# Optimization experiments

Hardware: AMD Instinct MI355X
Metric: run time of the kernel (lower is better)

Reference implementation:

```python
import jax, jax.numpy as jnp
import numpy as np

H, W, D = 56, 56, 28            # input_resolution
WS = (7, 7, 7)                  # window size (Wh, Ww, Wd)
SS = (3, 3, 3)                  # shift size
DIM = 96
NH = 3
HD = DIM // NH
N = WS[0] * WS[1] * WS[2]       # 343 tokens per window
NW = (H // WS[0]) * (W // WS[1]) * (D // WS[2])  # 256 windows


def _rel_pos_index():
    Wd, Wh, Ww = WS
    coords = np.stack(np.meshgrid(np.arange(Wd), np.arange(Wh), np.arange(Ww), indexing='ij'))
    cf = coords.reshape(3, -1)
    rel = (cf[:, :, None] - cf[:, None, :]).transpose(1, 2, 0)
    rel[:, :, 0] += Wd - 1
    rel[:, :, 1] += Wh - 1
    rel[:, :, 2] += Ww - 1
    rel[:, :, 0] *= (2 * Wh - 1) * (2 * Ww - 1)
    rel[:, :, 1] *= (2 * Ww - 1)
    return rel.sum(-1)  # (N, N)


def _attn_mask():
    img = np.zeros((H, W, D), np.float32)
    def slices(w, s):
        return (slice(0, -w), slice(-w, -s), slice(-s, None))
    cnt = 0
    for hs in slices(WS[0], SS[0]):
        for ws in slices(WS[1], SS[1]):
            for ds in slices(WS[2], SS[2]):
                img[hs, ws, ds] = cnt
                cnt += 1
    mw = img.reshape(H // WS[0], WS[0], W // WS[1], WS[1], D // WS[2], WS[2])
    mw = mw.transpose(0, 2, 4, 1, 3, 5).reshape(-1, N)  # (NW, N)
    am = mw[:, None, :] - mw[:, :, None]
    return np.where(am != 0, np.float32(-100.0), np.float32(0.0))


REL_IDX = jnp.asarray(_rel_pos_index())
ATTN_MASK = jnp.asarray(_attn_mask())  # (NW, N, N)


def _ln(x, g, b, eps=1e-5):
    m = x.mean(-1, keepdims=True)
    v = jnp.mean((x - m) ** 2, -1, keepdims=True)
    return (x - m) * jax.lax.rsqrt(v + eps) * g + b


def _forward(x, n1g, n1b, qkv_w, qkv_b, rpb, proj_w, proj_b,
             n2g, n2b, fc1_w, fc1_b, fc2_w, fc2_b):
    B, L, C = x.shape
    shortcut = x
    h = _ln(x, n1g, n1b).reshape(B, H, W, D, C)
    # cyclic shift
    h = jnp.roll(h, (-SS[0], -SS[1], -SS[2]), axis=(1, 2, 3))
    # window partition -> (B*NW, N, C)
    h = h.reshape(B, H // WS[0], WS[0], W // WS[1], WS[1], D // WS[2], WS[2], C)
    h = h.transpose(0, 1, 3, 5, 2, 4, 6, 7).reshape(-1, N, C)
    # qkv
    qkv = (h @ qkv_w + qkv_b).reshape(-1, N, 3, NH, HD).transpose(2, 0, 3, 1, 4)
    q, k, v = qkv[0] * (HD ** -0.5), qkv[1], qkv[2]  # (B*NW, NH, N, HD)
    attn = jnp.einsum('bhnd,bhmd->bhnm', q, k)
    bias = rpb[REL_IDX.reshape(-1)].reshape(N, N, NH).transpose(2, 0, 1)
    attn = attn + bias[None]
    # shifted-window mask
    attn = attn.reshape(B, NW, NH, N, N) + ATTN_MASK[None, :, None]
    attn = jax.nn.softmax(attn.reshape(-1, NH, N, N), axis=-1)
    o = jnp.einsum('bhnm,bhmd->bhnd', attn, v).transpose(0, 2, 1, 3).reshape(-1, N, C)
    o = o @ proj_w + proj_b
    # window reverse
    o = o.reshape(B, H // WS[0], W // WS[1], D // WS[2], WS[0], WS[1], WS[2], C)
    o = o.transpose(0, 1, 4, 2, 5, 3, 6, 7).reshape(B, H, W, D, C)
    o = jnp.roll(o, SS, axis=(1, 2, 3)).reshape(B, L, C)
    x = shortcut + o
    h2 = _ln(x, n2g, n2b)
    h2 = jax.nn.gelu(h2 @ fc1_w + fc1_b, approximate=False) @ fc2_w + fc2_b
    return x + h2


def setup_inputs() -> dict:
    key = jax.random.key(0)
    ks = jax.random.split(key, 6)
    C, FF = DIM, 4 * DIM
    f32 = jnp.float32
    return {
        'x': jax.random.normal(ks[0], (1, H * W * D, C), f32),
        'n1g': jnp.ones((C,), f32), 'n1b': jnp.zeros((C,), f32),
        'qkv_w': jax.random.normal(ks[1], (C, 3 * C), f32) * 0.02,
        'qkv_b': jnp.zeros((3 * C,), f32),
        'rpb': jax.random.normal(ks[2], ((2 * WS[0] - 1) * (2 * WS[1] - 1) * (2 * WS[2] - 1), NH), f32) * 0.02,
        'proj_w': jax.random.normal(ks[3], (C, C), f32) * 0.02,
        'proj_b': jnp.zeros((C,), f32),
        'n2g': jnp.ones((C,), f32), 'n2b': jnp.zeros((C,), f32),
        'fc1_w': jax.random.normal(ks[4], (C, FF), f32) * 0.02,
        'fc1_b': jnp.zeros((FF,), f32),
        'fc2_w': jax.random.normal(ks[5], (FF, C), f32) * 0.02,
        'fc2_b': jnp.zeros((C,), f32),
    }


def reference(x, n1g, n1b, qkv_w, qkv_b, rpb, proj_w, proj_b,
              n2g, n2b, fc1_w, fc1_b, fc2_w, fc2_b):
    return _forward(x, n1g, n1b, qkv_w, qkv_b, rpb, proj_w, proj_b,
                    n2g, n2b, fc1_w, fc1_b, fc2_w, fc2_b)
```

## Files before the change

kernel.cpp:

```cpp
#include <hip/hip_runtime.h>
#include <hip/hip_bf16.h>


#define L_TOK 87808

typedef unsigned int uint;
typedef __attribute__((ext_vector_type(8))) short short8;
typedef __attribute__((ext_vector_type(4))) float f32x4;

__device__ __forceinline__ float bflo(uint u){ union{uint x; float f;} a; a.x = u << 16; return a.f; }
__device__ __forceinline__ float bfhi(uint u){ union{uint x; float f;} a; a.x = u & 0xffff0000u; return a.f; }
__device__ __forceinline__ float bfval(unsigned short w){ union{uint x; float f;} a; a.x = (uint)w << 16; return a.f; }
__device__ __forceinline__ unsigned short f2bfbits(float f){
  union{float f; uint u;} a; a.f = f;
  uint u = a.u;
  u += 0x7fffu + ((u >> 16) & 1u);
  return (unsigned short)(u >> 16);
}
__device__ __forceinline__ unsigned short bfb(float f){
  __hip_bfloat16 h = __float2bfloat16(f);
  return *reinterpret_cast<unsigned short*>(&h);
}
__device__ __forceinline__ uint pkbf(float a, float b){
  return ((uint)bfb(b) << 16) | (uint)bfb(a);
}
__device__ __forceinline__ uint pack2(float a, float b){
  return ((uint)f2bfbits(b) << 16) | (uint)f2bfbits(a);
}
__device__ __forceinline__ uint4 pack8(const float* p){
  uint4 u;
  u.x = pack2(p[0], p[1]); u.y = pack2(p[2], p[3]);
  u.z = pack2(p[4], p[5]); u.w = pack2(p[6], p[7]);
  return u;
}
__device__ __forceinline__ uint4 pack8g(const float* gp){
  float t[8];
  *(float4*)&t[0] = *(const float4*)gp;
  *(float4*)&t[4] = *(const float4*)(gp + 4);
  return pack8(t);
}

__global__ __launch_bounds__(256)
void k_tr(const float* __restrict__ src, unsigned short* __restrict__ dst,
          int K, int N)
{
  const int idx = blockIdx.x * 256 + threadIdx.x;
  if (idx < K * N) {
    const int n = idx / K, k = idx % K;
    dst[idx] = f2bfbits(src[(size_t)k * N + n]);
  }
}

__global__ __launch_bounds__(256)
void k_mb(const float* __restrict__ rpbg, unsigned short* __restrict__ MB)
{
  const int idx = blockIdx.x * 256 + threadIdx.x;
  const int cls = idx / (3*352*352);
  const int rem = idx - cls * (3*352*352);
  const int h = rem / (352*352);
  const int rem2 = rem - h * (352*352);
  const int q = rem2 / 352;
  const int k = rem2 - q * 352;
  unsigned short v = 0xFF80;
  if (q < 343 && k < 343) {
    const int q0 = q/49, q1 = (q%49)/7, q2 = q%7;
    const int k0 = k/49, k1 = (k%49)/7, k2 = k%7;
    const int bq = q0*169 + q1*13 + q2;
    const int bk = k0*169 + k1*13 + k2;
    float bias = rpbg[(size_t)(bq - bk + 1098)*3 + h];
    int cq = 0, ck = 0;
    if (cls & 4) { cq += ((q0 < 4) ? 1 : 2)*9; ck += ((k0 < 4) ? 1 : 2)*9; }
    if (cls & 2) { cq += ((q1 < 4) ? 1 : 2)*3; ck += ((k1 < 4) ? 1 : 2)*3; }
    if (cls & 1) { cq += (q2 < 4) ? 1 : 2;     ck += (k2 < 4) ? 1 : 2; }
    if (cq != ck) bias -= 100.0f;
    v = f2bfbits(bias);
  }
  MB[idx] = v;
}

__global__ __launch_bounds__(256)
void k_qkv_ln(const float* __restrict__ x,
              const float* __restrict__ n1g,
              const float* __restrict__ n1b,
              const unsigned short* __restrict__ qkvwt,
              const float* __restrict__ bias, size_t headStride,
              __hip_bfloat16* __restrict__ qb,
              __hip_bfloat16* __restrict__ kb,
              __hip_bfloat16* __restrict__ vb)
{
  __shared__ __align__(16) unsigned short As[64][104];
  __shared__ uint srcOff[64];
  __shared__ float gLds[96], bLds[96];
  __shared__ float pSum[256], pSq[256];
  __shared__ float mLds[64], sLds[64];

  const int tid = threadIdx.x;
  const int wave = tid >> 6, lane = tid & 63;
  const int row0 = blockIdx.x * 64;
  const int h = (int)blockIdx.y;
  __hip_bfloat16* qh = qb + (size_t)h * headStride;
  __hip_bfloat16* kh = kb + (size_t)h * headStride;
  __hip_bfloat16* vh = vb + (size_t)h * headStride;

  if (tid < 64) {
    const uint row = (uint)(row0 + tid);
    const uint win = row / 343u, n = row % 343u;
    const uint wh = win >> 5, ww = (win >> 2) & 7u, wd = win & 3u;
    const uint ih = n / 49u, rr = n % 49u, iw = rr / 7u, id = rr % 7u;
    uint gh = wh*7u + ih + 3u; if (gh >= 56u) gh -= 56u;
    uint gw = ww*7u + iw + 3u; if (gw >= 56u) gw -= 56u;
    uint gd = wd*7u + id + 3u; if (gd >= 28u) gd -= 28u;
    srcOff[tid] = ((gh*56u + gw)*28u + gd) * 96u;
  }
  if (tid < 96) { gLds[tid] = n1g[tid]; bLds[tid] = n1b[tid]; }
  __syncthreads();

  for (int i = tid; i < 768; i += 256) {
    const int r = i / 12, kk = (i % 12) * 8;
    *(uint4*)&As[r][kk] = pack8g(x + srcOff[r] + kk);
  }
  __syncthreads();

  {
    const int r = tid & 63, seg = tid >> 6;
    float s = 0.0f, sq = 0.0f;
    #pragma unroll
    for (int j = 0; j < 24; ++j) {
      const float v = bfval(As[r][seg*24 + j]);
      s += v; sq += v*v;
    }
    pSum[tid] = s; pSq[tid] = sq;
  }
  __syncthreads();
  if (tid < 64) {
    const float s  = pSum[tid] + pSum[tid+64] + pSum[tid+128] + pSum[tid+192];
    const float sq = pSq[tid] + pSq[tid+64] + pSq[tid+128] + pSq[tid+192];
    const float mean = s * (1.0f/96.0f);
    mLds[tid] = mean;
    sLds[tid] = rsqrtf(sq*(1.0f/96.0f) - mean*mean + 1e-5f);
  }
  __syncthreads();
  for (int i = tid; i < 768; i += 256) {
    const int r = i / 12, kk = (i % 12) * 8;
    uint4 u = *(uint4*)&As[r][kk];
    const float m = mLds[r], sc = sLds[r];
    float v[8];
    v[0]=bflo(u.x); v[1]=bfhi(u.x); v[2]=bflo(u.y); v[3]=bfhi(u.y);
    v[4]=bflo(u.z); v[5]=bfhi(u.z); v[6]=bflo(u.w); v[7]=bfhi(u.w);
    #pragma unroll
    for (int j = 0; j < 8; ++j) v[j] = (v[j] - m)*sc*gLds[kk+j] + bLds[kk+j];
    *(uint4*)&As[r][kk] = pack8(v);
  }
  __syncthreads();

  f32x4 acc[6];
  #pragma unroll
  for (int i = 0; i < 6; ++i) acc[i] = (f32x4){0.f, 0.f, 0.f, 0.f};
  const int ml = lane & 15, q8 = (lane >> 4) * 8;
  #pragma unroll
  for (int nt = 0; nt < 6; ++nt) {
    const int col = nt*16 + ml;
    const int wcol = (col >> 5)*96 + h*32 + (col & 31);
    #pragma unroll
    for (int kc = 0; kc < 3; ++kc) {
      const short8 a = *(const short8*)&As[wave*16 + ml][kc*32 + q8];
      const short8 b = *(const short8*)(qkvwt + (size_t)wcol*96 + kc*32 + q8);
      acc[nt] = __builtin_amdgcn_mfma_f32_16x16x32_bf16(a, b, acc[nt], 0, 0, 0);
    }
  }

  const float qscale = 0.17677669529663687f;
  #pragma unroll
  for (int r = 0; r < 4; ++r) {
    const size_t row = (size_t)(row0 + wave*16 + (lane >> 4)*4 + r);
    #pragma unroll
    for (int nt = 0; nt < 6; ++nt) {
      const int col = nt*16 + ml;
      const int part = col >> 5, d = col & 31;
      float v = acc[nt][r] + bias[part*96 + h*32 + d];
      if (part == 0) v *= qscale;
      __hip_bfloat16* dst = (part == 0) ? qh : ((part == 1) ? kh : vh);
      dst[row*32 + d] = __float2bfloat16(v);
    }
  }
}

__global__ __launch_bounds__(256, 4)
void k_attn_v10(const __hip_bfloat16* __restrict__ qg,
                const __hip_bfloat16* __restrict__ kg,
                const __hip_bfloat16* __restrict__ vg,
                size_t headStride,
                const unsigned short* __restrict__ MB,
                float* __restrict__ ob)
{
  __shared__ __align__(16) unsigned short vt[32*344 + 16];
  __shared__ __align__(16) unsigned short Pc[4][16*56];
  __shared__ float lred[4][16];

  const int tid = threadIdx.x;
  const int wave = tid >> 6, lane = tid & 63;
  const uint win = blockIdx.x;
  const int hh = (int)blockIdx.y;
  const int mtBase = (int)blockIdx.z * 11;
  const size_t wbase = (size_t)hh * headStride + (size_t)win * (343*32);
  const unsigned short* qw = (const unsigned short*)qg + wbase;
  const unsigned short* kw = (const unsigned short*)kg + wbase;
  const unsigned short* vw = (const unsigned short*)vg + wbase;

  const uint wh = win >> 5, ww = (win >> 2) & 7u, wd = win & 3u;
  const int cls = ((wh == 7u) ? 4 : 0) | ((ww == 7u) ? 2 : 0) | ((wd == 3u) ? 1 : 0);
  const unsigned short* MBh = MB + ((size_t)cls*3 + hh) * (352*352);

  for (int t = tid; t < 343; t += 256) {
    const uint4* src = (const uint4*)(vw + (size_t)t*32);
    #pragma unroll
    for (int c4 = 0; c4 < 4; ++c4) {
      const uint4 u = src[c4];
      const int d = c4*8;
      vt[(d+0)*344 + t] = (unsigned short)(u.x & 0xffffu);
      vt[(d+1)*344 + t] = (unsigned short)(u.x >> 16);
      vt[(d+2)*344 + t] = (unsigned short)(u.y & 0xffffu);
      vt[(d+3)*344 + t] = (unsigned short)(u.y >> 16);
      vt[(d+4)*344 + t] = (unsigned short)(u.z & 0xffffu);
      vt[(d+5)*344 + t] = (unsigned short)(u.z >> 16);
      vt[(d+6)*344 + t] = (unsigned short)(u.w & 0xffffu);
      vt[(d+7)*344 + t] = (unsigned short)(u.w >> 16);
    }
  }
  if (tid < 32) vt[tid*344 + 343] = 0;
  if (tid < 16) vt[32*344 + tid] = 0;
  __syncthreads();

  const int ml = lane & 15, g = lane >> 4, g8 = g*8;
  unsigned short* Pw = &Pc[wave][0];

  for (int mt = mtBase + wave; mt < mtBase + 11; mt += 4) {
    const int q = mt*16 + ml;
    const short8 qf = *(const short8*)(qw + (size_t)q*32 + g8);
    const unsigned short* MBq = MBh + (size_t)q * 352;
    float l = 0.0f;
    f32x4 o0 = {0.f,0.f,0.f,0.f}, o1 = {0.f,0.f,0.f,0.f};

    for (int kc = 0; kc < 11; ++kc) {
      const short8 kf0 = *(const short8*)(kw + (size_t)(kc*32 + ml)*32 + g8);
      const short8 kf1 = *(const short8*)(kw + (size_t)(kc*32 + 16 + ml)*32 + g8);
      f32x4 s0 = __builtin_amdgcn_mfma_f32_16x16x32_bf16(kf0, qf, (f32x4){0.f,0.f,0.f,0.f}, 0, 0, 0);
      f32x4 s1 = __builtin_amdgcn_mfma_f32_16x16x32_bf16(kf1, qf, (f32x4){0.f,0.f,0.f,0.f}, 0, 0, 0);

      const ushort4 u0 = *(const ushort4*)(MBq + kc*32 + 4*g);
      const ushort4 u1 = *(const ushort4*)(MBq + kc*32 + 16 + 4*g);

      float p0 = __expf(s0[0] + bfval(u0.x));
      float p1 = __expf(s0[1] + bfval(u0.y));
      float p2 = __expf(s0[2] + bfval(u0.z));
      float p3 = __expf(s0[3] + bfval(u0.w));
      float p4 = __expf(s1[0] + bfval(u1.x));
      float p5 = __expf(s1[1] + bfval(u1.y));
      float p6 = __expf(s1[2] + bfval(u1.z));
      float p7 = __expf(s1[3] + bfval(u1.w));
      l += ((p0 + p1) + (p2 + p3)) + ((p4 + p5) + (p6 + p7));

      uint2 wlo, whi;
      wlo.x = pkbf(p0, p1); wlo.y = pkbf(p2, p3);
      whi.x = pkbf(p4, p5); whi.y = pkbf(p6, p7);
      *(uint2*)&Pw[ml*56 + 4*g]      = wlo;
      *(uint2*)&Pw[ml*56 + 16 + 4*g] = whi;

      const short8 pf  = *(const short8*)&Pw[ml*56 + g8];
      const short8 vf0 = *(const short8*)&vt[(size_t)ml*344 + kc*32 + g8];
      const short8 vf1 = *(const short8*)&vt[(size_t)(16 + ml)*344 + kc*32 + g8];
      o0 = __builtin_amdgcn_mfma_f32_16x16x32_bf16(pf, vf0, o0, 0, 0, 0);
      o1 = __builtin_amdgcn_mfma_f32_16x16x32_bf16(pf, vf1, o1, 0, 0, 0);
    }

    l += __shfl_xor(l, 16);
    l += __shfl_xor(l, 32);
    if (g == 0) lred[wave][ml] = 1.0f / l;
    const float4 li = *(const float4*)&lred[wave][4*g];
    #pragma unroll
    for (int r = 0; r < 4; ++r) {
      const int row = mt*16 + 4*g + r;
      if (row < 343) {
        float* op = ob + ((size_t)win*343 + (uint)row)*96 + hh*32;
        op[ml]      = o0[r] * li[r];
        op[16 + ml] = o1[r] * li[r];
      }
    }
  }
}

__global__ __launch_bounds__(256, 4)
void k_attn_v9(const __hip_bfloat16* __restrict__ qg,
               const __hip_bfloat16* __restrict__ kg,
               const __hip_bfloat16* __restrict__ vg,
               size_t headStride,
               const float* __restrict__ rpbg,
               float* __restrict__ ob)
{
  __shared__ __align__(16) unsigned short vt[32*344 + 16];
  __shared__ __align__(16) unsigned short Pc[4][16*40];
  __shared__ short baseT[352];
  __shared__ unsigned char cntT[352];
  __shared__ unsigned short rpB[2197];

  const int tid = threadIdx.x;
  const int wave = tid >> 6, lane = tid & 63;
  const uint win = blockIdx.x;
  const int hh = (int)blockIdx.y;
  const int mtBase = (int)blockIdx.z * 11;
  const size_t wbase = (size_t)hh * headStride + (size_t)win * (343*32);
  const unsigned short* qw = (const unsigned short*)qg + wbase;
  const unsigned short* kw = (const unsigned short*)kg + wbase;
  const unsigned short* vw = (const unsigned short*)vg + wbase;

  for (int i = tid; i < 2197; i += 256) rpB[i] = f2bfbits(rpbg[i*3 + hh]);
  const uint wh = win >> 5, ww = (win >> 2) & 7u, wd = win & 3u;
  for (int i = tid; i < 352; i += 256) {
    if (i < 343) {
      const uint c0 = (uint)i/49u, rr = (uint)i%49u, c1 = rr/7u, c2 = rr%7u;
      baseT[i] = (short)(c0*169u + c1*13u + c2);
      const uint g0 = wh*7u + c0, g1 = ww*7u + c1, g2 = wd*7u + c2;
      const uint rh = (g0 < 49u) ? 0u : ((g0 < 53u) ? 1u : 2u);
      const uint rw = (g1 < 49u) ? 0u : ((g1 < 53u) ? 1u : 2u);
      const uint rd = (g2 < 21u) ? 0u : ((g2 < 25u) ? 1u : 2u);
      cntT[i] = (unsigned char)(rh*9u + rw*3u + rd);
    } else { baseT[i] = 0; cntT[i] = 255; }
  }
  for (int t = tid; t < 343; t += 256) {
    const uint4* src = (const uint4*)(vw + (size_t)t*32);
    #pragma unroll
    for (int c4 = 0; c4 < 4; ++c4) {
      const uint4 u = src[c4];
      const int d = c4*8;
      vt[(d+0)*344 + t] = (unsigned short)(u.x & 0xffffu);
      vt[(d+1)*344 + t] = (unsigned short)(u.x >> 16);
      vt[(d+2)*344 + t] = (unsigned short)(u.y & 0xffffu);
      vt[(d+3)*344 + t] = (unsigned short)(u.y >> 16);
      vt[(d+4)*344 + t] = (unsigned short)(u.z & 0xffffu);
      vt[(d+5)*344 + t] = (unsigned short)(u.z >> 16);
      vt[(d+6)*344 + t] = (unsigned short)(u.w & 0xffffu);
      vt[(d+7)*344 + t] = (unsigned short)(u.w >> 16);
    }
  }
  if (tid < 32) vt[tid*344 + 343] = 0;
  if (tid < 16) vt[32*344 + tid] = 0;
  __syncthreads();

  const int ml = lane & 15, g = lane >> 4, g8 = g*8;
  unsigned short* Pw = &Pc[wave][0];

  for (int mt = mtBase + wave; mt < mtBase + 11; mt += 4) {
    const int qrow = mt*16;
    const short8 qf = *(const short8*)(qw + (size_t)(qrow + ml)*32 + g8);
    int cnR[4], biR[4];
    #pragma unroll
    for (int r = 0; r < 4; ++r) {
      const int gi = qrow + g*4 + r;
      cnR[r] = (int)cntT[gi];
      biR[r] = (int)baseT[gi] + 1098;
    }
    float m_[4], l_[4];
    #pragma unroll
    for (int r = 0; r < 4; ++r) { m_[r] = -1e30f; l_[r] = 0.0f; }
    f32x4 o0 = {0.f,0.f,0.f,0.f}, o1 = {0.f,0.f,0.f,0.f};

    for (int kc = 0; kc < 11; ++kc) {
      const int c0 = kc*32 + ml, c1 = c0 + 16;
      const short8 kf0 = *(const short8*)(kw + (size_t)c0*32 + g8);
      const short8 kf1 = *(const short8*)(kw + (size_t)c1*32 + g8);
      f32x4 s0 = __builtin_amdgcn_mfma_f32_16x16x32_bf16(qf, kf0, (f32x4){0.f,0.f,0.f,0.f}, 0, 0, 0);
      f32x4 s1 = __builtin_amdgcn_mfma_f32_16x16x32_bf16(qf, kf1, (f32x4){0.f,0.f,0.f,0.f}, 0, 0, 0);

      float bv0[4], bv1[4];
      const int bj0 = (int)baseT[c0], bj1 = (int)baseT[c1];
      #pragma unroll
      for (int r = 0; r < 4; ++r) {
        bv0[r] = bfval(rpB[biR[r] - bj0]);
        bv1[r] = bfval(rpB[biR[r] - bj1]);
      }
      const int cj0 = (int)cntT[c0], cj1 = (int)cntT[c1];

      float a_[4];
      #pragma unroll
      for (int r = 0; r < 4; ++r) {
        float v0 = s0[r] + bv0[r];
        float v1 = s1[r] + bv1[r];
        v0 += (cj0 == cnR[r]) ? 0.0f : -100.0f;
        v1 += (cj1 == cnR[r]) ? 0.0f : -100.0f;
        v1 = (c1 < 343) ? v1 : -1e30f;
        s0[r] = v0; s1[r] = v1;
        float cm = fmaxf(v0, v1);
        cm = fmaxf(cm, __shfl_xor(cm, 1));
        cm = fmaxf(cm, __shfl_xor(cm, 2));
        cm = fmaxf(cm, __shfl_xor(cm, 4));
        cm = fmaxf(cm, __shfl_xor(cm, 8));
        const float mn = fmaxf(m_[r], cm);
        a_[r] = __expf(m_[r] - mn);
        m_[r] = mn;
      }
      #pragma unroll
      for (int r = 0; r < 4; ++r) {
        const float p0 = __expf(s0[r] - m_[r]);
        const float p1 = __expf(s1[r] - m_[r]);
        Pw[(g*4 + r)*40 + ml]      = f2bfbits(p0);
        Pw[(g*4 + r)*40 + 16 + ml] = f2bfbits(p1);
        float cs = p0 + p1;
        cs += __shfl_xor(cs, 1);
        cs += __shfl_xor(cs, 2);
        cs += __shfl_xor(cs, 4);
        cs += __shfl_xor(cs, 8);
        l_[r] = l_[r]*a_[r] + cs;
        o0[r] *= a_[r];
        o1[r] *= a_[r];
      }
      const short8 pf  = *(const short8*)&Pw[ml*40 + g8];
      const short8 vf0 = *(const short8*)&vt[(size_t)ml*344 + kc*32 + g8];
      const short8 vf1 = *(const short8*)&vt[(size_t)(16 + ml)*344 + kc*32 + g8];
      o0 = __builtin_amdgcn_mfma_f32_16x16x32_bf16(pf, vf0, o0, 0, 0, 0);
      o1 = __builtin_amdgcn_mfma_f32_16x16x32_bf16(pf, vf1, o1, 0, 0, 0);
    }

    #pragma unroll
    for (int r = 0; r < 4; ++r) {
      const int row = qrow + g*4 + r;
      if (row < 343) {
        const float inv = 1.0f / l_[r];
        float* op = ob + ((size_t)win*343 + (uint)row)*96 + hh*32;
        op[ml]      = o0[r] * inv;
        op[16 + ml] = o1[r] * inv;
      }
    }
  }
}

__global__ __launch_bounds__(256)
void k_proj(const float* __restrict__ A,
            const unsigned short* __restrict__ pwt,
            const float* __restrict__ bias,
            const float* __restrict__ xin,
            __hip_bfloat16* __restrict__ xres)
{
  __shared__ __align__(16) unsigned short As[64][104];
  const int tid = threadIdx.x;
  const int wave = tid >> 6, lane = tid & 63;
  const int row0 = blockIdx.x * 64;

  for (int i = tid; i < 768; i += 256) {
    const int r = i / 12, kk = (i % 12) * 8;
    *(uint4*)&As[r][kk] = pack8g(A + (size_t)(row0 + r)*96 + kk);
  }
  __syncthreads();

  f32x4 acc[6];
  #pragma unroll
  for (int i = 0; i < 6; ++i) acc[i] = (f32x4){0.f, 0.f, 0.f, 0.f};
  const int ml = lane & 15, q8 = (lane >> 4) * 8;
  #pragma unroll
  for (int kc = 0; kc < 3; ++kc) {
    const short8 a = *(const short8*)&As[wave*16 + ml][kc*32 + q8];
    #pragma unroll
    for (int nt = 0; nt < 6; ++nt) {
      const short8 b = *(const short8*)(pwt + (size_t)(nt*16 + ml)*96 + kc*32 + q8);
      acc[nt] = __builtin_amdgcn_mfma_f32_16x16x32_bf16(a, b, acc[nt], 0, 0, 0);
    }
  }

  #pragma unroll
  for (int r = 0; r < 4; ++r) {
    const uint row = (uint)(row0 + wave*16 + (lane >> 4)*4 + r);
    const uint win = row / 343u, n = row % 343u;
    const uint wh = win >> 5, ww = (win >> 2) & 7u, wd = win & 3u;
    const uint ih = n / 49u, rr = n % 49u, iw = rr / 7u, id = rr % 7u;
    uint gh = wh*7u + ih + 3u; if (gh >= 56u) gh -= 56u;
    uint gw = ww*7u + iw + 3u; if (gw >= 56u) gw -= 56u;
    uint gd = wd*7u + id + 3u; if (gd >= 28u) gd -= 28u;
    const size_t gt = (size_t)((gh*56u + gw)*28u + gd) * 96;
    #pragma unroll
    for (int nt = 0; nt < 6; ++nt) {
      const int col = nt*16 + ml;
      xres[gt + col] = __float2bfloat16(acc[nt][r] + bias[col] + xin[gt + col]);
    }
  }
}

__global__ __launch_bounds__(256)
void k_mlp(const __hip_bfloat16* __restrict__ xresb,
           const float* __restrict__ n2g,
           const float* __restrict__ n2b,
           const unsigned short* __restrict__ w1t,
           const float* __restrict__ b1,
           const unsigned short* __restrict__ w2t,
           const float* __restrict__ b2,
           float* __restrict__ out)
{
  __shared__ __align__(16) unsigned short As[32][104];
  __shared__ __align__(16) unsigned short inter[32][392];
  __shared__ float gLds[96], bLds[96];
  __shared__ float pSum[256], pSq[256];
  __shared__ float mLds[32], sLds[32];
  const int tid = threadIdx.x;
  const int wave = tid >> 6, lane = tid & 63;
  const int row0 = blockIdx.x * 32;
  const int ml = lane & 15, q8 = (lane >> 4) * 8;
  const int mt = (wave * 3) / 6;
  const int nt0 = (wave * 3) % 6;

  if (tid < 96) { gLds[tid] = n2g[tid]; bLds[tid] = n2b[tid]; }
  for (int i = tid; i < 384; i += 256) {
    const int r = i / 12, kk = (i % 12) * 8;
    *(uint4*)&As[r][kk] = *(const uint4*)(xresb + (size_t)(row0 + r)*96 + kk);
  }
  __syncthreads();

  {
    const int r = tid & 31, seg = tid >> 5;
    float s = 0.0f, sq = 0.0f;
    #pragma unroll
    for (int j = 0; j < 12; ++j) {
      const float v = bfval(As[r][seg*12 + j]);
      s += v; sq += v*v;
    }
    pSum[tid] = s; pSq[tid] = sq;
  }
  __syncthreads();
  if (tid < 32) {
    float s = 0.0f, sq = 0.0f;
    #pragma unroll
    for (int k = 0; k < 8; ++k) { s += pSum[tid + 32*k]; sq += pSq[tid + 32*k]; }
    const float mean = s * (1.0f/96.0f);
    mLds[tid] = mean;
    sLds[tid] = rsqrtf(sq*(1.0f/96.0f) - mean*mean + 1e-5f);
  }
  __syncthreads();
  for (int i = tid; i < 384; i += 256) {
    const int r = i / 12, kk = (i % 12) * 8;
    uint4 u = *(uint4*)&As[r][kk];
    const float m = mLds[r], sc = sLds[r];
    float v[8];
    v[0]=bflo(u.x); v[1]=bfhi(u.x); v[2]=bflo(u.y); v[3]=bfhi(u.y);
    v[4]=bflo(u.z); v[5]=bfhi(u.z); v[6]=bflo(u.w); v[7]=bfhi(u.w);
    #pragma unroll
    for (int j = 0; j < 8; ++j) v[j] = (v[j] - m)*sc*gLds[kk+j] + bLds[kk+j];
    *(uint4*)&As[r][kk] = pack8(v);
  }
  __syncthreads();

  for (int ny = 0; ny < 4; ++ny) {
    f32x4 acc[3];
    #pragma unroll
    for (int i = 0; i < 3; ++i) acc[i] = (f32x4){0.f, 0.f, 0.f, 0.f};
    #pragma unroll
    for (int kc = 0; kc < 3; ++kc) {
      const short8 a = *(const short8*)&As[mt*16 + ml][kc*32 + q8];
      #pragma unroll
      for (int i = 0; i < 3; ++i) {
        const int n = ny*96 + (nt0 + i)*16 + ml;
        const short8 b = *(const short8*)(w1t + (size_t)n*96 + kc*32 + q8);
        acc[i] = __builtin_amdgcn_mfma_f32_16x16x32_bf16(a, b, acc[i], 0, 0, 0);
      }
    }
    #pragma unroll
    for (int i = 0; i < 3; ++i) {
      #pragma unroll
      for (int r = 0; r < 4; ++r) {
        const int row = mt*16 + (lane >> 4)*4 + r;
        const int col = ny*96 + (nt0 + i)*16 + ml;
        float v = acc[i][r] + b1[col];
        v = 0.5f * v * (1.0f + erff(v * 0.70710678118654752f));
        inter[row][col] = f2bfbits(v);
      }
    }
  }
  __syncthreads();

  f32x4 acc2[3];
  #pragma unroll
  for (int i = 0; i < 3; ++i) acc2[i] = (f32x4){0.f, 0.f, 0.f, 0.f};
  for (int kc = 0; kc < 12; ++kc) {
    const short8 a = *(const short8*)&inter[mt*16 + ml][kc*32 + q8];
    #pragma unroll
    for (int i = 0; i < 3; ++i) {
      const int n = (nt0 + i)*16 + ml;
      const short8 b = *(const short8*)(w2t + (size_t)n*384 + kc*32 + q8);
      acc2[i] = __builtin_amdgcn_mfma_f32_16x16x32_bf16(a, b, acc2[i], 0, 0, 0);
    }
  }

  const unsigned short* xu = (const unsigned short*)xresb;
  #pragma unroll
  for (int i = 0; i < 3; ++i) {
    #pragma unroll
    for (int r = 0; r < 4; ++r) {
      const size_t row = (size_t)(row0 + mt*16 + (lane >> 4)*4 + r);
      const int col = (nt0 + i)*16 + ml;
      out[row*96 + col] = acc2[i][r] + b2[col] + bfval(xu[row*96 + col]);
    }
  }
}

extern "C" void kernel_launch(void* const* d_in, const int* in_sizes, int n_in,
                              void* d_out, int out_size, void* d_ws, size_t ws_size,
                              hipStream_t stream)
{
  (void)in_sizes; (void)n_in; (void)out_size;
  const float* x    = (const float*)d_in[0];
  const float* n1g  = (const float*)d_in[1];
  const float* n1b  = (const float*)d_in[2];
  const float* qkvw = (const float*)d_in[3];
  const float* qkvb = (const float*)d_in[4];
  const float* rpb  = (const float*)d_in[5];
  const float* pw   = (const float*)d_in[6];
  const float* pb   = (const float*)d_in[7];
  const float* n2g  = (const float*)d_in[8];
  const float* n2b  = (const float*)d_in[9];
  const float* f1w  = (const float*)d_in[10];
  const float* f1b  = (const float*)d_in[11];
  const float* f2w  = (const float*)d_in[12];
  const float* f2b  = (const float*)d_in[13];
  float* out = (float*)d_out;

  const size_t E = (size_t)L_TOK * 96;
  __hip_bfloat16* qb = (__hip_bfloat16*)d_ws;
  __hip_bfloat16* kb = qb + E;
  __hip_bfloat16* vb = kb + E;
  __hip_bfloat16* xres = (__hip_bfloat16*)d_ws;
  float* ob = out;
  const size_t hs = (size_t)L_TOK * 32;

  unsigned short* qkvwt = (unsigned short*)d_out;
  unsigned short* pwt   = (unsigned short*)kb;
  unsigned short* w1t   = pwt + 9216;
  unsigned short* w2t   = w1t + 36864;

  const size_t MB_BYTES = (size_t)8 * 3 * 352 * 352 * 2;
  unsigned short* MBp = nullptr;
  if (ws_size >= (size_t)6 * E + MB_BYTES) {
    MBp = (unsigned short*)((char*)d_ws + (size_t)6 * E);
    k_mb<<<11616, 256, 0, stream>>>(rpb, MBp);
  }

  k_tr<<<108, 256, 0, stream>>>(qkvw, qkvwt, 96, 288);
  k_qkv_ln<<<dim3(L_TOK/64, 3), 256, 0, stream>>>(
      x, n1g, n1b, qkvwt, qkvb, hs, qb, kb, vb);
  if (MBp)
    k_attn_v10<<<dim3(256, 3, 2), 256, 0, stream>>>(qb, kb, vb, hs, MBp, ob);
  else
    k_attn_v9<<<dim3(256, 3, 2), 256, 0, stream>>>(qb, kb, vb, hs, rpb, ob);
  k_tr<<<36, 256, 0, stream>>>(pw, pwt, 96, 96);
  k_tr<<<144, 256, 0, stream>>>(f1w, w1t, 96, 384);
  k_tr<<<144, 256, 0, stream>>>(f2w, w2t, 384, 96);
  k_proj<<<L_TOK/64, 256, 0, stream>>>(ob, pwt, pb, x, xres);
  k_mlp<<<L_TOK/32, 256, 0, stream>>>(xres, n2g, n2b, w1t, f1b, w2t, f2b, out);
}
```

Before: 310.6 us.

## Retile MLP kernel to 64-row blocks with register-cached A/B fragments

```diff
diff --git a/kernel.cpp b/kernel.cpp
--- a/kernel.cpp
+++ b/kernel.cpp
@@ -158,12 +158,12 @@
   for (int i = 0; i < 6; ++i) acc[i] = (f32x4){0.f, 0.f, 0.f, 0.f};
   const int ml = lane & 15, q8 = (lane >> 4) * 8;
   #pragma unroll
-  for (int nt = 0; nt < 6; ++nt) {
-    const int col = nt*16 + ml;
-    const int wcol = (col >> 5)*96 + h*32 + (col & 31);
-    #pragma unroll
-    for (int kc = 0; kc < 3; ++kc) {
-      const short8 a = *(const short8*)&As[wave*16 + ml][kc*32 + q8];
+  for (int kc = 0; kc < 3; ++kc) {
+    const short8 a = *(const short8*)&As[wave*16 + ml][kc*32 + q8];
+    #pragma unroll
+    for (int nt = 0; nt < 6; ++nt) {
+      const int col = nt*16 + ml;
+      const int wcol = (col >> 5)*96 + h*32 + (col & 31);
       const short8 b = *(const short8*)(qkvwt + (size_t)wcol*96 + kc*32 + q8);
       acc[nt] = __builtin_amdgcn_mfma_f32_16x16x32_bf16(a, b, acc[nt], 0, 0, 0);
     }
@@ -483,7 +483,7 @@
   }
 }
 
-__global__ __launch_bounds__(256)
+__global__ __launch_bounds__(256, 2)
 void k_mlp(const __hip_bfloat16* __restrict__ xresb,
            const float* __restrict__ n2g,
            const float* __restrict__ n2b,
@@ -493,107 +493,146 @@
            const float* __restrict__ b2,
            float* __restrict__ out)
 {
-  __shared__ __align__(16) unsigned short As[32][104];
-  __shared__ __align__(16) unsigned short inter[32][392];
-  __shared__ float gLds[96], bLds[96];
-  __shared__ float pSum[256], pSq[256];
-  __shared__ float mLds[32], sLds[32];
+  __shared__ __align__(16) unsigned short As[64][104];
+  __shared__ __align__(16) unsigned short inter[64][392];
+  float* scr  = (float*)&inter[0][0];
+  float* pSum = scr;
+  float* pSq  = scr + 256;
+  float* gL   = scr + 512;
+  float* bL   = scr + 608;
+  float* mL   = scr + 704;
+  float* sL   = scr + 768;
+
   const int tid = threadIdx.x;
   const int wave = tid >> 6, lane = tid & 63;
-  const int row0 = blockIdx.x * 32;
-  const int ml = lane & 15, q8 = (lane >> 4) * 8;
-  const int mt = (wave * 3) / 6;
-  const int nt0 = (wave * 3) % 6;
-
-  if (tid < 96) { gLds[tid] = n2g[tid]; bLds[tid] = n2b[tid]; }
-  for (int i = tid; i < 384; i += 256) {
+  const int row0 = blockIdx.x * 64;
+  const int ml = lane & 15, g = lane >> 4, g8 = g*8;
+
+  if (tid < 96) { gL[tid] = n2g[tid]; bL[tid] = n2b[tid]; }
+  for (int i = tid; i < 768; i += 256) {
     const int r = i / 12, kk = (i % 12) * 8;
     *(uint4*)&As[r][kk] = *(const uint4*)(xresb + (size_t)(row0 + r)*96 + kk);
   }
   __syncthreads();
 
   {
-    const int r = tid & 31, seg = tid >> 5;
+    const int r = tid & 63, seg = tid >> 6;
     float s = 0.0f, sq = 0.0f;
     #pragma unroll
-    for (int j = 0; j < 12; ++j) {
-      const float v = bfval(As[r][seg*12 + j]);
-      s += v; sq += v*v;
+    for (int j3 = 0; j3 < 3; ++j3) {
+      const uint4 u = *(const uint4*)&As[r][seg*24 + j3*8];
+      float v[8];
+      v[0]=bflo(u.x); v[1]=bfhi(u.x); v[2]=bflo(u.y); v[3]=bfhi(u.y);
+      v[4]=bflo(u.z); v[5]=bfhi(u.z); v[6]=bflo(u.w); v[7]=bfhi(u.w);
+      #pragma unroll
+      for (int j = 0; j < 8; ++j) { s += v[j]; sq += v[j]*v[j]; }
     }
     pSum[tid] = s; pSq[tid] = sq;
   }
   __syncthreads();
-  if (tid < 32) {
-    float s = 0.0f, sq = 0.0f;
-    #pragma unroll
-    for (int k = 0; k < 8; ++k) { s += pSum[tid + 32*k]; sq += pSq[tid + 32*k]; }
+  if (tid < 64) {
+    const float s  = pSum[tid] + pSum[tid+64] + pSum[tid+128] + pSum[tid+192];
+    const float sq = pSq[tid] + pSq[tid+64] + pSq[tid+128] + pSq[tid+192];
     const float mean = s * (1.0f/96.0f);
-    mLds[tid] = mean;
-    sLds[tid] = rsqrtf(sq*(1.0f/96.0f) - mean*mean + 1e-5f);
-  }
-  __syncthreads();
-  for (int i = tid; i < 384; i += 256) {
+    mL[tid] = mean;
+    sL[tid] = rsqrtf(sq*(1.0f/96.0f) - mean*mean + 1e-5f);
+  }
+  __syncthreads();
+  for (int i = tid; i < 768; i += 256) {
     const int r = i / 12, kk = (i % 12) * 8;
     uint4 u = *(uint4*)&As[r][kk];
-    const float m = mLds[r], sc = sLds[r];
+    const float m = mL[r], sc = sL[r];
     float v[8];
     v[0]=bflo(u.x); v[1]=bfhi(u.x); v[2]=bflo(u.y); v[3]=bfhi(u.y);
     v[4]=bflo(u.z); v[5]=bfhi(u.z); v[6]=bflo(u.w); v[7]=bfhi(u.w);
     #pragma unroll
-    for (int j = 0; j < 8; ++j) v[j] = (v[j] - m)*sc*gLds[kk+j] + bLds[kk+j];
+    for (int j = 0; j < 8; ++j) v[j] = (v[j] - m)*sc*gL[kk+j] + bL[kk+j];
     *(uint4*)&As[r][kk] = pack8(v);
   }
   __syncthreads();
 
-  for (int ny = 0; ny < 4; ++ny) {
-    f32x4 acc[3];
-    #pragma unroll
-    for (int i = 0; i < 3; ++i) acc[i] = (f32x4){0.f, 0.f, 0.f, 0.f};
-    #pragma unroll
-    for (int kc = 0; kc < 3; ++kc) {
-      const short8 a = *(const short8*)&As[mt*16 + ml][kc*32 + q8];
-      #pragma unroll
-      for (int i = 0; i < 3; ++i) {
-        const int n = ny*96 + (nt0 + i)*16 + ml;
-        const short8 b = *(const short8*)(w1t + (size_t)n*96 + kc*32 + q8);
-        acc[i] = __builtin_amdgcn_mfma_f32_16x16x32_bf16(a, b, acc[i], 0, 0, 0);
+  short8 af[4][3];
+  #pragma unroll
+  for (int mt = 0; mt < 4; ++mt)
+    #pragma unroll
+    for (int kc = 0; kc < 3; ++kc)
+      af[mt][kc] = *(const short8*)&As[mt*16 + ml][kc*32 + g8];
+
+  const int nb = 96 * wave;
+  #pragma unroll
+  for (int ny = 0; ny < 2; ++ny) {
+    short8 bf[3][3];
+    #pragma unroll
+    for (int nt = 0; nt < 3; ++nt)
+      #pragma unroll
+      for (int kc = 0; kc < 3; ++kc)
+        bf[nt][kc] = *(const short8*)(w1t + (size_t)(nb + 48*ny + 16*nt + ml)*96 + kc*32 + g8);
+
+    f32x4 acc[4][3];
+    #pragma unroll
+    for (int mt = 0; mt < 4; ++mt)
+      #pragma unroll
+      for (int nt = 0; nt < 3; ++nt)
+        acc[mt][nt] = (f32x4){0.f, 0.f, 0.f, 0.f};
+
+    #pragma unroll
+    for (int kc = 0; kc < 3; ++kc)
+      #pragma unroll
+      for (int nt = 0; nt < 3; ++nt)
+        #pragma unroll
+        for (int mt = 0; mt < 4; ++mt)
+          acc[mt][nt] = __builtin_amdgcn_mfma_f32_16x16x32_bf16(af[mt][kc], bf[nt][kc], acc[mt][nt], 0, 0, 0);
+
+    #pragma unroll
+    for (int nt = 0; nt < 3; ++nt) {
+      const int col = nb + 48*ny + 16*nt + ml;
+      const float b1v = b1[col];
+      #pragma unroll
+      for (int mt = 0; mt < 4; ++mt) {
+        #pragma unroll
+        for (int r = 0; r < 4; ++r) {
+          float v = acc[mt][nt][r] + b1v;
+          v = 0.5f * v * (1.0f + erff(v * 0.70710678118654752f));
+          inter[mt*16 + 4*g + r][col] = f2bfbits(v);
+        }
       }
     }
-    #pragma unroll
-    for (int i = 0; i < 3; ++i) {
+  }
+  __syncthreads();
+
+  const int rb = 32 * (wave >> 1);
+  const int cb = 48 * (wave & 1);
+  f32x4 acc2[2][3];
+  #pragma unroll
+  for (int i = 0; i < 2; ++i)
+    #pragma unroll
+    for (int nt = 0; nt < 3; ++nt)
+      acc2[i][nt] = (f32x4){0.f, 0.f, 0.f, 0.f};
+
+  #pragma unroll
+  for (int kc = 0; kc < 12; ++kc) {
+    short8 a0 = *(const short8*)&inter[rb + ml][kc*32 + g8];
+    short8 a1 = *(const short8*)&inter[rb + 16 + ml][kc*32 + g8];
+    #pragma unroll
+    for (int nt = 0; nt < 3; ++nt) {
+      const short8 b = *(const short8*)(w2t + (size_t)(cb + 16*nt + ml)*384 + kc*32 + g8);
+      acc2[0][nt] = __builtin_amdgcn_mfma_f32_16x16x32_bf16(a0, b, acc2[0][nt], 0, 0, 0);
+      acc2[1][nt] = __builtin_amdgcn_mfma_f32_16x16x32_bf16(a1, b, acc2[1][nt], 0, 0, 0);
+    }
+  }
+
+  const unsigned short* xu = (const unsigned short*)xresb;
+  #pragma unroll
+  for (int i = 0; i < 2; ++i) {
+    #pragma unroll
+    for (int nt = 0; nt < 3; ++nt) {
+      const int col = cb + 16*nt + ml;
+      const float b2v = b2[col];
       #pragma unroll
       for (int r = 0; r < 4; ++r) {
-        const int row = mt*16 + (lane >> 4)*4 + r;
-        const int col = ny*96 + (nt0 + i)*16 + ml;
-        float v = acc[i][r] + b1[col];
-        v = 0.5f * v * (1.0f + erff(v * 0.70710678118654752f));
-        inter[row][col] = f2bfbits(v);
+        const size_t row = (size_t)(row0 + rb + 16*i + 4*g + r);
+        out[row*96 + col] = acc2[i][nt][r] + b2v + bfval(xu[row*96 + col]);
       }
-    }
-  }
-  __syncthreads();
-
-  f32x4 acc2[3];
-  #pragma unroll
-  for (int i = 0; i < 3; ++i) acc2[i] = (f32x4){0.f, 0.f, 0.f, 0.f};
-  for (int kc = 0; kc < 12; ++kc) {
-    const short8 a = *(const short8*)&inter[mt*16 + ml][kc*32 + q8];
-    #pragma unroll
-    for (int i = 0; i < 3; ++i) {
-      const int n = (nt0 + i)*16 + ml;
-      const short8 b = *(const short8*)(w2t + (size_t)n*384 + kc*32 + q8);
-      acc2[i] = __builtin_amdgcn_mfma_f32_16x16x32_bf16(a, b, acc2[i], 0, 0, 0);
-    }
-  }
-
-  const unsigned short* xu = (const unsigned short*)xresb;
-  #pragma unroll
-  for (int i = 0; i < 3; ++i) {
-    #pragma unroll
-    for (int r = 0; r < 4; ++r) {
-      const size_t row = (size_t)(row0 + mt*16 + (lane >> 4)*4 + r);
-      const int col = (nt0 + i)*16 + ml;
-      out[row*96 + col] = acc2[i][r] + b2[col] + bfval(xu[row*96 + col]);
     }
   }
 }
@@ -650,5 +689,5 @@
   k_tr<<<144, 256, 0, stream>>>(f1w, w1t, 96, 384);
   k_tr<<<144, 256, 0, stream>>>(f2w, w2t, 384, 96);
   k_proj<<<L_TOK/64, 256, 0, stream>>>(ob, pwt, pb, x, xres);
-  k_mlp<<<L_TOK/32, 256, 0, stream>>>(xres, n2g, n2b, w1t, f1b, w2t, f2b, out);
-}
+  k_mlp<<<L_TOK/64, 256, 0, stream>>>(xres, n2g, n2b, w1t, f1b, w2t, f2b, out);
+}
```

Result: faster. 294.9 us (-5.0%).
